# Performance work log

Measured on AMD Instinct MI355X. Metric: run time of the kernel, lower is better.

The kernel has to match this reference:

```python
import jax, jax.numpy as jnp
import numpy as np

DEC_HIDDEN = 512


def setup_inputs() -> dict:
    key = jax.random.key(0)
    k1, k2, k3, k4 = jax.random.split(key, 4)
    B, S, DEC, ENC2 = 32, 2048, 512, 1024
    s = jax.random.normal(k1, (1, B, DEC), dtype=jnp.float32)
    enc_output = jax.random.normal(k2, (B, S, ENC2), dtype=jnp.float32)
    # nn.Linear weights: attn [dec_hidden, enc_hidden*2 + dec_hidden], v [1, dec_hidden]
    W_attn = jax.random.normal(k3, (DEC, DEC + ENC2), dtype=jnp.float32) * (1.0 / np.sqrt(DEC + ENC2))
    W_v = jax.random.normal(k4, (1, DEC), dtype=jnp.float32) * (1.0 / np.sqrt(DEC))
    return {"s": s, "enc_output": enc_output, "W_attn": W_attn, "W_v": W_v}


def reference(s, enc_output, W_attn, W_v):
    # s: [1, B, D] -> [B, D]; enc_output: [B, S, 2E]
    s = jnp.squeeze(s, axis=0)
    dec = s.shape[-1]
    # torch.cat((s_repeated, enc_output), dim=2) @ W_attn.T, computed without
    # materializing the repeat/concat: split W_attn by column blocks.
    W_s = W_attn[:, :dec]       # [D, D]   (columns matching s)
    W_e = W_attn[:, dec:]       # [D, 2E]  (columns matching enc_output)
    # energy: [B, S, D]
    energy = jnp.tanh(
        jnp.einsum('bd,hd->bh', s, W_s)[:, None, :]
        + jnp.einsum('bse,he->bsh', enc_output, W_e)
    )
    # atten: [B, S]
    atten = jnp.einsum('bsh,h->bs', energy, W_v[0])
    soft_attn_weights = jax.nn.softmax(atten, axis=1)
    # context: [B, 2E]
    context = jnp.einsum('bs,bse->be', soft_attn_weights, enc_output)
    return (context, soft_attn_weights)
```

## Files before the change

kernel.cpp:

```cpp
#include <hip/hip_runtime.h>
#include <hip/hip_bf16.h>


typedef __attribute__((ext_vector_type(8))) short bf16x8;
typedef __attribute__((ext_vector_type(4))) float f32x4;

#define SB0() __builtin_amdgcn_sched_barrier(0)

static __device__ __forceinline__ unsigned short f2bf(float f) {
    union { float f; unsigned u; } v; v.f = f;
    unsigned r = (v.u + 0x7fffu + ((v.u >> 16) & 1u)) >> 16;
    return (unsigned short)r;
}

static __device__ __forceinline__ unsigned pk2(float x, float y) {
    union { __hip_bfloat162 h; unsigned u; } c;
    c.h = __float22bfloat162_rn(make_float2(x, y));
    return c.u;
}

static __device__ __forceinline__ float fast_tanh(float x) {
    return 1.0f - 2.0f / (__expf(2.0f * x) + 1.0f);
}

__global__ __launch_bounds__(256) void prep_sw(const float* __restrict__ s,
                                               const float* __restrict__ Wat,
                                               float* __restrict__ sW) {
    int id = blockIdx.x * 256 + threadIdx.x;
    int b = id >> 9, h = id & 511;
    const float4* wr = (const float4*)(Wat + (size_t)h * 1536);
    const float4* sr = (const float4*)(s + (size_t)b * 512);
    float acc = 0.f;
#pragma unroll 8
    for (int i = 0; i < 128; ++i) {
        float4 w = wr[i], sv = sr[i];
        acc += w.x * sv.x + w.y * sv.y + w.z * sv.z + w.w * sv.w;
    }
    sW[id] = acc;
}

__global__ __launch_bounds__(256) void prep_weB(const float* __restrict__ Wat,
                                                unsigned short* __restrict__ WebfB) {
    int tid = blockIdx.x * 256 + threadIdx.x;
    int lane = tid & 63;
    int g = tid >> 6;
    int nf = g & 3, wc = (g >> 2) & 3, kk = (g >> 4) & 1, step = (g >> 5) & 15, ct = (g >> 9) & 1;
    int col = ct * 256 + wc * 64 + nf * 16 + (lane & 15);
    int k0 = step * 64 + kk * 32 + (lane >> 4) * 8;
    const float* src = Wat + (size_t)col * 1536 + 512 + k0;
    float4 w0 = *(const float4*)src;
    float4 w1 = *(const float4*)(src + 4);
    union { unsigned short us[8]; int4 v; } p;
    p.us[0] = f2bf(w0.x); p.us[1] = f2bf(w0.y); p.us[2] = f2bf(w0.z); p.us[3] = f2bf(w0.w);
    p.us[4] = f2bf(w1.x); p.us[5] = f2bf(w1.y); p.us[6] = f2bf(w1.z); p.us[7] = f2bf(w1.w);
    *(int4*)(WebfB + (size_t)tid * 8) = p.v;
}

__global__ __launch_bounds__(512, 2) void energy_kernel(
    const float* __restrict__ enc, const unsigned short* __restrict__ WebfB,
    const float* __restrict__ sW, const float* __restrict__ Wv,
    float* __restrict__ attpart) {
    __shared__ __align__(16) unsigned short lT0[8192];
    __shared__ __align__(16) unsigned short lT1[8192];
    __shared__ float lred[8][64];

    const int t = threadIdx.x;
    const int lane = t & 63;
    const int wave = t >> 6;
    const int wr = wave >> 2;
    const int wc = wave & 3;
    const int bid = blockIdx.x;
    const int ct = (bid >> 3) & 1;
    const int rt = (bid & 7) | ((bid >> 4) << 3);
    const int m0 = rt * 128;
    const int b = m0 >> 11;
    const int l15 = lane & 15;
    const int lkg = lane >> 4;

    const int arow = t >> 4;
    const int achk = t & 15;
    const float* aptr = enc + (size_t)(m0 + arow) * 1024 + achk * 4;
    const int wsw = (((achk >> 1) ^ (arow & 7)) << 4) | ((achk & 1) << 3);

    const int rrowbase = (wr * 64 + l15) * 128;
    const int rsw0 = (lkg ^ (l15 & 7)) << 4;
    const int rsw1 = ((4 + lkg) ^ (l15 & 7)) << 4;

    const unsigned short* wBbase = WebfB + (size_t)ct * 262144 + lane * 8;

    f32x4 acc[4][4];
#pragma unroll
    for (int mf = 0; mf < 4; ++mf)
#pragma unroll
        for (int nf = 0; nf < 4; ++nf) acc[mf][nf] = (f32x4){0.f, 0.f, 0.f, 0.f};

    float4 aregA[4], aregB[4];
    bf16x8 bfr[8];

#define LOADA(STEP, AR)                                                        \
    do {                                                                       \
        _Pragma("unroll")                                                      \
        for (int q = 0; q < 4; ++q)                                            \
            AR[q] = *(const float4*)(aptr + (size_t)q * 32768 + (STEP) * 64);  \
    } while (0)

#define LOADB(I)                                                               \
    do {                                                                       \
        _Pragma("unroll")                                                      \
        for (int kk = 0; kk < 2; ++kk)                                         \
            _Pragma("unroll")                                                  \
            for (int nf = 0; nf < 4; ++nf)                                     \
                bfr[kk * 4 + nf] = *(const bf16x8*)(                           \
                    wBbase + (size_t)((((I) * 2 + kk) * 4 + wc) * 4 + nf) * 512); \
    } while (0)

#define CVTW(AR, BUF)                                                          \
    do {                                                                       \
        _Pragma("unroll")                                                      \
        for (int q = 0; q < 4; ++q) {                                          \
            uint2 wv;                                                          \
            wv.x = pk2(AR[q].x, AR[q].y);                                      \
            wv.y = pk2(AR[q].z, AR[q].w);                                      \
            *(uint2*)((char*)(BUF) + (q * 32 + arow) * 128 + wsw) = wv;        \
        }                                                                      \
    } while (0)

#define COMP(BUF)                                                              \
    do {                                                                       \
        _Pragma("unroll")                                                      \
        for (int kk = 0; kk < 2; ++kk) {                                       \
            const int rs = kk ? rsw1 : rsw0;                                   \
            _Pragma("unroll")                                                  \
            for (int mf = 0; mf < 4; ++mf) {                                   \
                bf16x8 af = *(const bf16x8*)((const char*)(BUF) + rrowbase +   \
                                             mf * 2048 + rs);                  \
                _Pragma("unroll")                                              \
                for (int nf = 0; nf < 4; ++nf)                                 \
                    acc[mf][nf] = __builtin_amdgcn_mfma_f32_16x16x32_bf16(     \
                        af, bfr[kk * 4 + nf], acc[mf][nf], 0, 0, 0);           \
            }                                                                  \
        }                                                                      \
    } while (0)

#define BARRIER()                                              \
    do {                                                       \
        asm volatile("s_waitcnt lgkmcnt(0)" ::: "memory");     \
        __builtin_amdgcn_s_barrier();                          \
    } while (0)

#define STEP_FULL(I, CUR, NXT, AUSE, ALOAD)    \
    do {                                       \
        LOADB(I); SB0();                       \
        LOADA((I) + 2, ALOAD); SB0();          \
        CVTW(AUSE, NXT); SB0();                \
        __builtin_amdgcn_s_setprio(1);         \
        COMP(CUR);                             \
        __builtin_amdgcn_s_setprio(0);         \
        BARRIER();                             \
    } while (0)

    LOADA(0, aregA); SB0();
    LOADA(1, aregB); SB0();
    CVTW(aregA, lT0);
    BARRIER();

#pragma unroll 1
    for (int i = 0; i < 14; i += 2) {
        STEP_FULL(i, lT0, lT1, aregB, aregA);
        STEP_FULL(i + 1, lT1, lT0, aregA, aregB);
    }
    LOADB(14); SB0();
    CVTW(aregB, lT1); SB0();
    __builtin_amdgcn_s_setprio(1);
    COMP(lT0);
    __builtin_amdgcn_s_setprio(0);
    BARRIER();
    LOADB(15); SB0();
    __builtin_amdgcn_s_setprio(1);
    COMP(lT1);
    __builtin_amdgcn_s_setprio(0);

    float sWv[4], wvv[4];
#pragma unroll
    for (int nf = 0; nf < 4; ++nf) {
        int col = ct * 256 + wc * 64 + nf * 16 + l15;
        sWv[nf] = sW[(b << 9) + col];
        wvv[nf] = Wv[col];
    }
    float pa[4][4];
#pragma unroll
    for (int mf = 0; mf < 4; ++mf) {
#pragma unroll
        for (int r = 0; r < 4; ++r) pa[mf][r] = 0.f;
#pragma unroll
        for (int nf = 0; nf < 4; ++nf)
#pragma unroll
            for (int r = 0; r < 4; ++r)
                pa[mf][r] += fast_tanh(acc[mf][nf][r] + sWv[nf]) * wvv[nf];
    }
#pragma unroll
    for (int m = 1; m < 16; m <<= 1)
#pragma unroll
        for (int mf = 0; mf < 4; ++mf)
#pragma unroll
            for (int r = 0; r < 4; ++r)
                pa[mf][r] += __shfl_xor(pa[mf][r], m, 64);

    if (l15 == 0) {
#pragma unroll
        for (int mf = 0; mf < 4; ++mf)
#pragma unroll
            for (int r = 0; r < 4; ++r)
                lred[wave][mf * 16 + lkg * 4 + r] = pa[mf][r];
    }
    __syncthreads();
    if (t < 128) {
        int base = (t >> 6) * 4, rl = t & 63;
        attpart[(size_t)ct * 65536 + m0 + t] =
            (lred[base + 0][rl] + lred[base + 1][rl]) +
            (lred[base + 2][rl] + lred[base + 3][rl]);
    }
#undef LOADA
#undef LOADB
#undef CVTW
#undef COMP
#undef BARRIER
#undef STEP_FULL
}

__global__ __launch_bounds__(256) void softmax_kernel(const float* __restrict__ attpart,
                                                      float* __restrict__ out) {
    int b = blockIdx.x, t = threadIdx.x;
    float v[8];
#pragma unroll
    for (int i = 0; i < 8; ++i) {
        int idx = b * 2048 + t + 256 * i;
        v[i] = attpart[idx] + attpart[65536 + idx];
    }
    float mx = v[0];
#pragma unroll
    for (int i = 1; i < 8; ++i) mx = fmaxf(mx, v[i]);
#pragma unroll
    for (int m = 1; m < 64; m <<= 1) mx = fmaxf(mx, __shfl_xor(mx, m, 64));
    __shared__ float redm[4], reds[4];
    if ((t & 63) == 0) redm[t >> 6] = mx;
    __syncthreads();
    mx = fmaxf(fmaxf(redm[0], redm[1]), fmaxf(redm[2], redm[3]));
    float sum = 0.f;
#pragma unroll
    for (int i = 0; i < 8; ++i) { v[i] = __expf(v[i] - mx); sum += v[i]; }
#pragma unroll
    for (int m = 1; m < 64; m <<= 1) sum += __shfl_xor(sum, m, 64);
    if ((t & 63) == 0) reds[t >> 6] = sum;
    __syncthreads();
    sum = reds[0] + reds[1] + reds[2] + reds[3];
    float inv = 1.0f / sum;
    float* soft = out + 32768;
#pragma unroll
    for (int i = 0; i < 8; ++i) soft[b * 2048 + t + 256 * i] = v[i] * inv;
}

__global__ __launch_bounds__(256) void ctx_partial(const float* __restrict__ enc,
                                                   const float* __restrict__ soft,
                                                   float* __restrict__ part) {
    int blk = blockIdx.x;
    int b = blk >> 4, s0 = (blk & 15) * 128;
    int t = threadIdx.x;
    float4 a = {0.f, 0.f, 0.f, 0.f};
    const float* base = enc + ((size_t)(b * 2048 + s0)) * 1024 + t * 4;
    const float* sw = soft + b * 2048 + s0;
#pragma unroll 4
    for (int s = 0; s < 128; ++s) {
        float w = sw[s];
        float4 e = *(const float4*)(base + (size_t)s * 1024);
        a.x += w * e.x; a.y += w * e.y; a.z += w * e.z; a.w += w * e.w;
    }
    *(float4*)(part + (size_t)blk * 1024 + t * 4) = a;
}

__global__ __launch_bounds__(256) void ctx_reduce(const float* __restrict__ part,
                                                  float* __restrict__ ctx) {
    int id = blockIdx.x * 256 + threadIdx.x;
    int b = id >> 10, e = id & 1023;
    float s = 0.f;
#pragma unroll 8
    for (int c = 0; c < 16; ++c) s += part[((size_t)(b * 16 + c)) * 1024 + e];
    ctx[id] = s;
}

extern "C" void kernel_launch(void* const* d_in, const int* in_sizes, int n_in,
                              void* d_out, int out_size, void* d_ws, size_t ws_size,
                              hipStream_t stream) {
    const float* s   = (const float*)d_in[0];
    const float* enc = (const float*)d_in[1];
    const float* Wat = (const float*)d_in[2];
    const float* Wv  = (const float*)d_in[3];
    float* out = (float*)d_out;

    char* ws = (char*)d_ws;
    float* sW             = (float*)ws;
    unsigned short* WebfB = (unsigned short*)(ws + (64 << 10));
    float* attpart        = (float*)(ws + (64 << 10) + (1 << 20));
    float* part           = (float*)(ws + (64 << 10) + (1 << 20) + (512 << 10));

    prep_sw<<<64, 256, 0, stream>>>(s, Wat, sW);
    prep_weB<<<2048, 256, 0, stream>>>(Wat, WebfB);
    energy_kernel<<<1024, 512, 0, stream>>>(enc, WebfB, sW, Wv, attpart);
    softmax_kernel<<<32, 256, 0, stream>>>(attpart, out);
    ctx_partial<<<512, 256, 0, stream>>>(enc, out + 32768, part);
    ctx_reduce<<<128, 256, 0, stream>>>(part, out);
}
```

Baseline: 197.2 us.

## Stage fp32 encoder tiles directly into LDS and enlarge the energy tile

The energy GEMM kernel now copies fp32 encoder tiles straight from global memory into LDS with global_load_lds, instead of loading them into registers, converting to bf16 and writing them back. The fp32-to-bf16 conversion moves to after the LDS read, inside a four-phase schedule per K-step. Each phase interleaves the next tile's async loads, barriers and MFMAs. Each block now covers 256 rows instead of 128 with twice the accumulators, and the grid is halved. The aim is to cut register staging and VALU work on the load path and to raise B-fragment reuse. The cost is roughly 132 KB of LDS per block, which limits occupancy to one block per CU, plus heavier register pressure and more barriers. The prep_weB grid is also trimmed to match the number of elements it actually writes.

Result: slower. 207.2 us (+5.1%).

```diff
diff --git a/kernel.cpp b/kernel.cpp
--- a/kernel.cpp
+++ b/kernel.cpp
@@ -4,8 +4,12 @@
 
 typedef __attribute__((ext_vector_type(8))) short bf16x8;
 typedef __attribute__((ext_vector_type(4))) float f32x4;
+typedef __attribute__((address_space(3))) unsigned lds_u32;
+typedef const __attribute__((address_space(1))) unsigned g_u32;
 
 #define SB0() __builtin_amdgcn_sched_barrier(0)
+#define PRIO1 __builtin_amdgcn_s_setprio(1)
+#define PRIO0 __builtin_amdgcn_s_setprio(0)
 
 static __device__ __forceinline__ unsigned short f2bf(float f) {
     union { float f; unsigned u; } v; v.f = f;
@@ -60,9 +64,9 @@
     const float* __restrict__ enc, const unsigned short* __restrict__ WebfB,
     const float* __restrict__ sW, const float* __restrict__ Wv,
     float* __restrict__ attpart) {
-    __shared__ __align__(16) unsigned short lT0[8192];
-    __shared__ __align__(16) unsigned short lT1[8192];
-    __shared__ float lred[8][64];
+    __shared__ __align__(16) float buf0[16384];
+    __shared__ __align__(16) float buf1[16384];
+    __shared__ float lred[8][128];
 
     const int t = threadIdx.x;
     const int lane = t & 63;
@@ -72,113 +76,122 @@
     const int bid = blockIdx.x;
     const int ct = (bid >> 3) & 1;
     const int rt = (bid & 7) | ((bid >> 4) << 3);
-    const int m0 = rt * 128;
+    const int m0 = rt * 256;
     const int b = m0 >> 11;
     const int l15 = lane & 15;
     const int lkg = lane >> 4;
 
-    const int arow = t >> 4;
-    const int achk = t & 15;
-    const float* aptr = enc + (size_t)(m0 + arow) * 1024 + achk * 4;
-    const int wsw = (((achk >> 1) ^ (arow & 7)) << 4) | ((achk & 1) << 3);
-
-    const int rrowbase = (wr * 64 + l15) * 128;
-    const int rsw0 = (lkg ^ (l15 & 7)) << 4;
-    const int rsw1 = ((4 + lkg) ^ (l15 & 7)) << 4;
-
-    const unsigned short* wBbase = WebfB + (size_t)ct * 262144 + lane * 8;
-
-    f32x4 acc[4][4];
-#pragma unroll
-    for (int mf = 0; mf < 4; ++mf)
+    const int srow = wave * 4 + lkg;
+    const int r7s = srow & 7;
+    const float* gb0 = enc + (size_t)(m0 + srow) * 1024 + ((l15 ^ r7s) << 2);
+    const float* gb1 = gb0 + (size_t)128 * 1024;
+    const int so = wave * 256;
+
+    const int rbase = (wr * 128 + l15) * 64;
+    const int s00 = ((lkg * 2 + 0) ^ (l15 & 7)) << 2;
+    const int s01 = ((lkg * 2 + 1) ^ (l15 & 7)) << 2;
+    const int s10 = ((8 + lkg * 2 + 0) ^ (l15 & 7)) << 2;
+    const int s11 = ((8 + lkg * 2 + 1) ^ (l15 & 7)) << 2;
+
+    const unsigned short* wB = WebfB + (size_t)ct * 262144 + lane * 8;
+
+    f32x4 acc[8][4];
+#pragma unroll
+    for (int mf = 0; mf < 8; ++mf)
 #pragma unroll
         for (int nf = 0; nf < 4; ++nf) acc[mf][nf] = (f32x4){0.f, 0.f, 0.f, 0.f};
 
-    float4 aregA[4], aregB[4];
-    bf16x8 bfr[8];
-
-#define LOADA(STEP, AR)                                                        \
-    do {                                                                       \
-        _Pragma("unroll")                                                      \
-        for (int q = 0; q < 4; ++q)                                            \
-            AR[q] = *(const float4*)(aptr + (size_t)q * 32768 + (STEP) * 64);  \
-    } while (0)
-
-#define LOADB(I)                                                               \
+    bf16x8 bA[8], bB[8];
+
+#define STG(H, Q, SB, TILE)                                                    \
+    __builtin_amdgcn_global_load_lds(                                          \
+        (g_u32*)(((H) ? gb1 : gb0) + (size_t)(Q) * 32768 + (TILE) * 64),       \
+        (lds_u32*)((SB) + (H) * 8192 + (Q) * 2048 + so), 16, 0, 0)
+
+#define LOADB(I, BR)                                                           \
     do {                                                                       \
         _Pragma("unroll")                                                      \
         for (int kk = 0; kk < 2; ++kk)                                         \
             _Pragma("unroll")                                                  \
             for (int nf = 0; nf < 4; ++nf)                                     \
-                bfr[kk * 4 + nf] = *(const bf16x8*)(                           \
-                    wBbase + (size_t)((((I) * 2 + kk) * 4 + wc) * 4 + nf) * 512); \
+                BR[kk * 4 + nf] = *(const bf16x8*)(                            \
+                    wB + (size_t)(((I) * 2 + kk) * 16 + wc * 4 + nf) * 512);   \
     } while (0)
 
-#define CVTW(AR, BUF)                                                          \
+#define PHASE(MF0, RB, BCUR, STAGE_CODE, PRE_BAR)                              \
     do {                                                                       \
+        const float* p0 = (RB) + rbase + (MF0) * 1024;                         \
+        const float* p1 = p0 + 1024;                                           \
+        float4 v0 = *(const float4*)(p0 + s00);                                \
+        float4 v1 = *(const float4*)(p0 + s01);                                \
+        float4 v2 = *(const float4*)(p0 + s10);                                \
+        float4 v3 = *(const float4*)(p0 + s11);                                \
+        float4 v4 = *(const float4*)(p1 + s00);                                \
+        float4 v5 = *(const float4*)(p1 + s01);                                \
+        float4 v6 = *(const float4*)(p1 + s10);                                \
+        float4 v7 = *(const float4*)(p1 + s11);                                \
+        STAGE_CODE;                                                            \
+        PRE_BAR;                                                               \
+        __builtin_amdgcn_s_barrier();                                          \
+        union { unsigned u[4]; bf16x8 v; } a00, a01, a10, a11;                 \
+        a00.u[0] = pk2(v0.x, v0.y); a00.u[1] = pk2(v0.z, v0.w);                \
+        a00.u[2] = pk2(v1.x, v1.y); a00.u[3] = pk2(v1.z, v1.w);                \
+        a01.u[0] = pk2(v2.x, v2.y); a01.u[1] = pk2(v2.z, v2.w);                \
+        a01.u[2] = pk2(v3.x, v3.y); a01.u[3] = pk2(v3.z, v3.w);                \
+        a10.u[0] = pk2(v4.x, v4.y); a10.u[1] = pk2(v4.z, v4.w);                \
+        a10.u[2] = pk2(v5.x, v5.y); a10.u[3] = pk2(v5.z, v5.w);                \
+        a11.u[0] = pk2(v6.x, v6.y); a11.u[1] = pk2(v6.z, v6.w);                \
+        a11.u[2] = pk2(v7.x, v7.y); a11.u[3] = pk2(v7.z, v7.w);                \
+        PRIO1;                                                                 \
         _Pragma("unroll")                                                      \
-        for (int q = 0; q < 4; ++q) {                                          \
-            uint2 wv;                                                          \
-            wv.x = pk2(AR[q].x, AR[q].y);                                      \
-            wv.y = pk2(AR[q].z, AR[q].w);                                      \
-            *(uint2*)((char*)(BUF) + (q * 32 + arow) * 128 + wsw) = wv;        \
+        for (int nf = 0; nf < 4; ++nf) {                                       \
+            acc[MF0][nf] = __builtin_amdgcn_mfma_f32_16x16x32_bf16(            \
+                a00.v, BCUR[nf], acc[MF0][nf], 0, 0, 0);                       \
+            acc[MF0][nf] = __builtin_amdgcn_mfma_f32_16x16x32_bf16(            \
+                a01.v, BCUR[4 + nf], acc[MF0][nf], 0, 0, 0);                   \
+            acc[(MF0) + 1][nf] = __builtin_amdgcn_mfma_f32_16x16x32_bf16(      \
+                a10.v, BCUR[nf], acc[(MF0) + 1][nf], 0, 0, 0);                 \
+            acc[(MF0) + 1][nf] = __builtin_amdgcn_mfma_f32_16x16x32_bf16(      \
+                a11.v, BCUR[4 + nf], acc[(MF0) + 1][nf], 0, 0, 0);             \
         }                                                                      \
+        PRIO0;                                                                 \
+        __builtin_amdgcn_s_barrier();                                          \
     } while (0)
 
-#define COMP(BUF)                                                              \
+#define VMC8() do { asm volatile("s_waitcnt vmcnt(8)" ::: "memory"); SB0(); } while (0)
+
+#define DO_TILE(I, RB, SB, BCUR, BNXT)                                         \
     do {                                                                       \
-        _Pragma("unroll")                                                      \
-        for (int kk = 0; kk < 2; ++kk) {                                       \
-            const int rs = kk ? rsw1 : rsw0;                                   \
-            _Pragma("unroll")                                                  \
-            for (int mf = 0; mf < 4; ++mf) {                                   \
-                bf16x8 af = *(const bf16x8*)((const char*)(BUF) + rrowbase +   \
-                                             mf * 2048 + rs);                  \
-                _Pragma("unroll")                                              \
-                for (int nf = 0; nf < 4; ++nf)                                 \
-                    acc[mf][nf] = __builtin_amdgcn_mfma_f32_16x16x32_bf16(     \
-                        af, bfr[kk * 4 + nf], acc[mf][nf], 0, 0, 0);           \
-            }                                                                  \
-        }                                                                      \
+        PHASE(0, RB, BCUR, { STG(0, 0, SB, (I) + 1); STG(0, 1, SB, (I) + 1); }, {}); \
+        PHASE(2, RB, BCUR, { STG(0, 2, SB, (I) + 1); STG(0, 3, SB, (I) + 1); }, {}); \
+        PHASE(4, RB, BCUR, { STG(1, 0, SB, (I) + 1); STG(1, 1, SB, (I) + 1); }, {}); \
+        PHASE(6, RB, BCUR,                                                     \
+              { STG(1, 2, SB, (I) + 1); STG(1, 3, SB, (I) + 1);                \
+                LOADB((I) + 1, BNXT); },                                       \
+              VMC8());                                                         \
     } while (0)
 
-#define BARRIER()                                              \
-    do {                                                       \
-        asm volatile("s_waitcnt lgkmcnt(0)" ::: "memory");     \
-        __builtin_amdgcn_s_barrier();                          \
+#define DO_TILE_LAST(RB, BCUR)                                                 \
+    do {                                                                       \
+        PHASE(0, RB, BCUR, {}, {});                                            \
+        PHASE(2, RB, BCUR, {}, {});                                            \
+        PHASE(4, RB, BCUR, {}, {});                                            \
+        PHASE(6, RB, BCUR, {}, {});                                            \
     } while (0)
 
-#define STEP_FULL(I, CUR, NXT, AUSE, ALOAD)    \
-    do {                                       \
-        LOADB(I); SB0();                       \
-        LOADA((I) + 2, ALOAD); SB0();          \
-        CVTW(AUSE, NXT); SB0();                \
-        __builtin_amdgcn_s_setprio(1);         \
-        COMP(CUR);                             \
-        __builtin_amdgcn_s_setprio(0);         \
-        BARRIER();                             \
-    } while (0)
-
-    LOADA(0, aregA); SB0();
-    LOADA(1, aregB); SB0();
-    CVTW(aregA, lT0);
-    BARRIER();
+    STG(0, 0, buf0, 0); STG(0, 1, buf0, 0); STG(0, 2, buf0, 0); STG(0, 3, buf0, 0);
+    STG(1, 0, buf0, 0); STG(1, 1, buf0, 0); STG(1, 2, buf0, 0); STG(1, 3, buf0, 0);
+    LOADB(0, bA);
+    VMC8();
+    __builtin_amdgcn_s_barrier();
 
 #pragma unroll 1
-    for (int i = 0; i < 14; i += 2) {
-        STEP_FULL(i, lT0, lT1, aregB, aregA);
-        STEP_FULL(i + 1, lT1, lT0, aregA, aregB);
-    }
-    LOADB(14); SB0();
-    CVTW(aregB, lT1); SB0();
-    __builtin_amdgcn_s_setprio(1);
-    COMP(lT0);
-    __builtin_amdgcn_s_setprio(0);
-    BARRIER();
-    LOADB(15); SB0();
-    __builtin_amdgcn_s_setprio(1);
-    COMP(lT1);
-    __builtin_amdgcn_s_setprio(0);
+    for (int k2 = 0; k2 < 7; ++k2) {
+        DO_TILE(2 * k2,     buf0, buf1, bA, bB);
+        DO_TILE(2 * k2 + 1, buf1, buf0, bB, bA);
+    }
+    DO_TILE(14, buf0, buf1, bA, bB);
+    DO_TILE_LAST(buf1, bB);
 
     float sWv[4], wvv[4];
 #pragma unroll
@@ -187,9 +200,9 @@
         sWv[nf] = sW[(b << 9) + col];
         wvv[nf] = Wv[col];
     }
-    float pa[4][4];
-#pragma unroll
-    for (int mf = 0; mf < 4; ++mf) {
+    float pa[8][4];
+#pragma unroll
+    for (int mf = 0; mf < 8; ++mf) {
 #pragma unroll
         for (int r = 0; r < 4; ++r) pa[mf][r] = 0.f;
 #pragma unroll
@@ -201,31 +214,31 @@
 #pragma unroll
     for (int m = 1; m < 16; m <<= 1)
 #pragma unroll
-        for (int mf = 0; mf < 4; ++mf)
+        for (int mf = 0; mf < 8; ++mf)
 #pragma unroll
             for (int r = 0; r < 4; ++r)
                 pa[mf][r] += __shfl_xor(pa[mf][r], m, 64);
 
     if (l15 == 0) {
 #pragma unroll
-        for (int mf = 0; mf < 4; ++mf)
+        for (int mf = 0; mf < 8; ++mf)
 #pragma unroll
             for (int r = 0; r < 4; ++r)
                 lred[wave][mf * 16 + lkg * 4 + r] = pa[mf][r];
     }
     __syncthreads();
-    if (t < 128) {
-        int base = (t >> 6) * 4, rl = t & 63;
-        attpart[(size_t)ct * 65536 + m0 + t] =
-            (lred[base + 0][rl] + lred[base + 1][rl]) +
-            (lred[base + 2][rl] + lred[base + 3][rl]);
-    }
-#undef LOADA
+    if (t < 256) {
+        int wrh = t >> 7, row = t & 127;
+        float ssum = (lred[wrh * 4 + 0][row] + lred[wrh * 4 + 1][row]) +
+                     (lred[wrh * 4 + 2][row] + lred[wrh * 4 + 3][row]);
+        attpart[(size_t)ct * 65536 + m0 + wrh * 128 + row] = ssum;
+    }
+#undef STG
 #undef LOADB
-#undef CVTW
-#undef COMP
-#undef BARRIER
-#undef STEP_FULL
+#undef PHASE
+#undef VMC8
+#undef DO_TILE
+#undef DO_TILE_LAST
 }
 
 __global__ __launch_bounds__(256) void softmax_kernel(const float* __restrict__ attpart,
@@ -304,8 +317,8 @@
     float* part           = (float*)(ws + (64 << 10) + (1 << 20) + (512 << 10));
 
     prep_sw<<<64, 256, 0, stream>>>(s, Wat, sW);
-    prep_weB<<<2048, 256, 0, stream>>>(Wat, WebfB);
-    energy_kernel<<<1024, 512, 0, stream>>>(enc, WebfB, sW, Wv, attpart);
+    prep_weB<<<256, 256, 0, stream>>>(Wat, WebfB);
+    energy_kernel<<<512, 512, 0, stream>>>(enc, WebfB, sW, Wv, attpart);
     softmax_kernel<<<32, 256, 0, stream>>>(attpart, out);
     ctx_partial<<<512, 256, 0, stream>>>(enc, out + 32768, part);
     ctx_reduce<<<128, 256, 0, stream>>>(part, out);
```
